# Performance work log

Measured on AMD Instinct MI355X. Metric: run time of the kernel, lower is better.

Reference implementation:

```python
import jax, jax.numpy as jnp
import numpy as np

N, E, IN, HID, OUT, H = 50000, 400000, 128, 32, 64, 4
HID_DIM = HID * H  # 128


def _param(key, shape, scale=0.05):
    return jax.random.normal(key, shape, dtype=jnp.float32) * scale


def setup_inputs() -> dict:
    key = jax.random.key(0)
    ks = jax.random.split(key, 32)
    inp = {
        "x": jax.random.normal(ks[0], (N, IN), dtype=jnp.float32),
        "edge_index": jax.random.randint(ks[1], (2, E), 0, N, dtype=jnp.int32),
        "edge_weight": jax.random.uniform(ks[2], (E,), dtype=jnp.float32),
        # layer 0: in=128 -> H=4, C=32, concat => 128
        "Wl0": _param(ks[3], (IN, H * HID)), "bl0": jnp.zeros((H * HID,), jnp.float32),
        "Wr0": _param(ks[4], (IN, H * HID)), "br0": jnp.zeros((H * HID,), jnp.float32),
        "We0": _param(ks[5], (1, H * HID)),
        "att0": _param(ks[6], (H, HID)),
        "b0": jnp.zeros((H * HID,), jnp.float32),
        "g0": jnp.ones((H * HID,), jnp.float32), "be0": jnp.zeros((H * HID,), jnp.float32),
        # layer 1: in=128 -> H=4, C=64, concat=False (mean over heads) => 64
        "Wl1": _param(ks[7], (HID_DIM, H * OUT)), "bl1": jnp.zeros((H * OUT,), jnp.float32),
        "Wr1": _param(ks[8], (HID_DIM, H * OUT)), "br1": jnp.zeros((H * OUT,), jnp.float32),
        "We1": _param(ks[9], (1, H * OUT)),
        "att1": _param(ks[10], (H, OUT)),
        "b1": jnp.zeros((OUT,), jnp.float32),
        "g1": jnp.ones((OUT,), jnp.float32), "be1": jnp.zeros((OUT,), jnp.float32),
        # residual projections
        "P0": _param(ks[11], (IN, HID_DIM)), "pb0": jnp.zeros((HID_DIM,), jnp.float32),
        "P1": _param(ks[12], (HID_DIM, OUT)), "pb1": jnp.zeros((OUT,), jnp.float32),
    }
    return inp


def _add_self_loops(src, dst, ew):
    # PyG add_self_loops with fill_value='mean': loop attr = mean of incoming edge attrs per node
    s = jax.ops.segment_sum(ew, dst, num_segments=N)
    cnt = jax.ops.segment_sum(jnp.ones_like(ew), dst, num_segments=N)
    loop_w = s / jnp.maximum(cnt, 1.0)
    idx = jnp.arange(N, dtype=src.dtype)
    return jnp.concatenate([src, idx]), jnp.concatenate([dst, idx]), jnp.concatenate([ew, loop_w])


def _gatv2_layer(x, src, dst, ew, Wl, bl, Wr, br, We, att, b, g, be, C, concat):
    xl = (x @ Wl + bl).reshape(N, H, C)  # source transform (lin_l)
    xr = (x @ Wr + br).reshape(N, H, C)  # target transform (lin_r)
    eattr = (ew[:, None] @ We).reshape(-1, H, C)
    e = jax.nn.leaky_relu(xl[src] + xr[dst] + eattr, 0.2)  # [E', H, C]
    logits = jnp.einsum('ehc,hc->eh', e, att)
    # segment softmax over target nodes
    m = jax.ops.segment_max(logits, dst, num_segments=N)
    p = jnp.exp(logits - m[dst])
    denom = jax.ops.segment_sum(p, dst, num_segments=N)
    alpha = p / denom[dst]
    out = jax.ops.segment_sum(xl[src] * alpha[..., None], dst, num_segments=N)  # [N, H, C]
    if concat:
        out = out.reshape(N, H * C) + b
    else:
        out = out.mean(axis=1) + b
    out = jax.nn.elu(out)
    mu = out.mean(-1, keepdims=True)
    var = out.var(-1, keepdims=True)
    return (out - mu) / jnp.sqrt(var + 1e-5) * g + be


def reference(x, edge_index, edge_weight,
              Wl0, bl0, Wr0, br0, We0, att0, b0, g0, be0,
              Wl1, bl1, Wr1, br1, We1, att1, b1, g1, be1,
              P0, pb0, P1, pb1):
    src, dst, ew = _add_self_loops(edge_index[0], edge_index[1], edge_weight)
    h = x
    h1 = _gatv2_layer(h, src, dst, ew, Wl0, bl0, Wr0, br0, We0, att0, b0, g0, be0, HID, True)
    h = h1 + (h @ P0 + pb0)
    h2 = _gatv2_layer(h, src, dst, ew, Wl1, bl1, Wr1, br1, We1, att1, b1, g1, be1, OUT, False)
    h = h2 + (h @ P1 + pb1)
    return h
```

## Files before the change

kernel.cpp:

```cpp
#include <hip/hip_runtime.h>
#include <math.h>

#define N_NODES 50000
#define N_EDGES 400000
#define NPAD    50176
#define MROWS   50048
#define HC0 128
#define HC1 256

typedef short    bf16x8 __attribute__((ext_vector_type(8)));
typedef float    f32x4  __attribute__((ext_vector_type(4)));
typedef _Float16 h2     __attribute__((ext_vector_type(2)));
typedef _Float16 h4     __attribute__((ext_vector_type(4)));
typedef _Float16 h8     __attribute__((ext_vector_type(8)));

__device__ inline unsigned short f2bf(float f) {
  union { float f; unsigned u; } v; v.f = f;
  unsigned r = v.u + 0x7FFFu + ((v.u >> 16) & 1u);
  return (unsigned short)(r >> 16);
}
__device__ inline h2 mkh2(float a, float b) {
  h2 r; r[0] = (_Float16)a; r[1] = (_Float16)b; return r;
}
__device__ inline float hdot2(h2 a, h2 b, float c) {
#if __has_builtin(__builtin_amdgcn_fdot2)
  return __builtin_amdgcn_fdot2(a, b, c, false);
#else
  return c + (float)a[0] * (float)b[0] + (float)a[1] * (float)b[1];
#endif
}

__global__ void deg_kernel(const int* __restrict__ ei, const float* __restrict__ ew,
                           float* __restrict__ s, int* __restrict__ deg) {
  int e = blockIdx.x * 256 + threadIdx.x;
  if (e < N_EDGES) {
    int dst = ei[N_EDGES + e];
    atomicAdd(&s[dst], ew[e]);
    atomicAdd(&deg[dst], 1);
  }
}

__global__ void scan1(const int* __restrict__ deg, int* __restrict__ part,
                      int* __restrict__ bsum) {
  int i = blockIdx.x * 256 + threadIdx.x;
  int lane = threadIdx.x & 63, wid = threadIdx.x >> 6;
  int v = (i < N_NODES) ? deg[i] + 1 : 0;
  int inc = v;
#pragma unroll
  for (int d = 1; d < 64; d <<= 1) { int y = __shfl_up(inc, d, 64); if (lane >= d) inc += y; }
  __shared__ int wsum[4];
  if (lane == 63) wsum[wid] = inc;
  __syncthreads();
  int off = 0;
#pragma unroll
  for (int w = 0; w < 4; ++w) { int sv = wsum[w]; if (w < wid) off += sv; }
  part[i] = inc - v + off;
  if (threadIdx.x == 0) bsum[blockIdx.x] = wsum[0] + wsum[1] + wsum[2] + wsum[3];
}

__global__ void scan2(int* __restrict__ bsum) {
  int t = threadIdx.x;
  int lane = t & 63, wid = t >> 6;
  int v = (t < 196) ? bsum[t] : 0;
  int inc = v;
#pragma unroll
  for (int d = 1; d < 64; d <<= 1) { int y = __shfl_up(inc, d, 64); if (lane >= d) inc += y; }
  __shared__ int wsum[4];
  if (lane == 63) wsum[wid] = inc;
  __syncthreads();
  int off = 0;
#pragma unroll
  for (int w = 0; w < 4; ++w) { int sv = wsum[w]; if (w < wid) off += sv; }
  if (t < 196) bsum[t] = inc - v + off;
}

__global__ void self_kernel(const float* __restrict__ s, const int* __restrict__ deg,
                            const int* __restrict__ part, const int* __restrict__ bsum,
                            int2* __restrict__ csr2) {
  int i = blockIdx.x * 256 + threadIdx.x;
  if (i >= N_NODES) return;
  float w = s[i] / fmaxf((float)deg[i], 1.0f);
  int start = part[i] + bsum[i >> 8];
  csr2[start] = make_int2(i, __float_as_int(w));
}

__global__ void scatter_kernel(const int* __restrict__ ei, const float* __restrict__ ew,
                               const int* __restrict__ part, const int* __restrict__ bsum,
                               int* __restrict__ cursor, int2* __restrict__ csr2) {
  int e = blockIdx.x * 256 + threadIdx.x;
  if (e >= N_EDGES) return;
  int dst = ei[N_EDGES + e];
  int pos = atomicAdd(&cursor[dst], 1);
  int idx = part[dst] + bsum[dst >> 8] + 1 + pos;
  csr2[idx] = make_int2(ei[e], __float_as_int(ew[e]));
}

__global__ void cvt_bf16(const float* __restrict__ in, unsigned short* __restrict__ out,
                         int n4) {
  int i = blockIdx.x * 256 + threadIdx.x;
  if (i >= n4) return;
  float4 v = ((const float4*)in)[i];
  ushort4 o; o.x = f2bf(v.x); o.y = f2bf(v.y); o.z = f2bf(v.z); o.w = f2bf(v.w);
  ((ushort4*)out)[i] = o;
}

__global__ void pack_w(const float* __restrict__ Wl0, const float* __restrict__ Wr0,
                       const float* __restrict__ P0,  const float* __restrict__ Wl1,
                       const float* __restrict__ Wr1, const float* __restrict__ P1,
                       unsigned short* __restrict__ o_wl0, unsigned short* __restrict__ o_wr0,
                       unsigned short* __restrict__ o_p0,  unsigned short* __restrict__ o_wl1,
                       unsigned short* __restrict__ o_wr1, unsigned short* __restrict__ o_p1) {
  int n = blockIdx.x, k = threadIdx.x;
  const float* W; unsigned short* O; int N, nl;
  if      (n < 128) { W = Wl0; O = o_wl0; N = 128; nl = n; }
  else if (n < 256) { W = Wr0; O = o_wr0; N = 128; nl = n - 128; }
  else if (n < 384) { W = P0;  O = o_p0;  N = 128; nl = n - 256; }
  else if (n < 640) { W = Wl1; O = o_wl1; N = 256; nl = n - 384; }
  else if (n < 896) { W = Wr1; O = o_wr1; N = 256; nl = n - 640; }
  else              { W = P1;  O = o_p1;  N = 64;  nl = n - 896; }
  O[nl * 128 + k] = f2bf(W[(size_t)k * N + nl]);
}

__global__ __launch_bounds__(256) void gemm_l0(
    const unsigned short* __restrict__ A, const unsigned short* __restrict__ BT,
    const float* __restrict__ bias0, const float* __restrict__ bias1,
    const float* __restrict__ bias2,
    _Float16* __restrict__ o_xl, _Float16* __restrict__ o_xr,
    float* __restrict__ o_h, int M) {
  __shared__ unsigned short As[64 * 136];
  const int tid = threadIdx.x;
  const int rbase = blockIdx.x * 64;
#pragma unroll
  for (int i = 0; i < 4; ++i) {
    int c = i * 256 + tid;
    int row = c >> 4, slot = c & 15;
    int ar = rbase + row; if (ar > M - 1) ar = M - 1;
    uint4 v = *(const uint4*)(A + (size_t)ar * 128 + slot * 8);
    *(uint4*)(As + row * 136 + slot * 8) = v;
  }
  __syncthreads();
  const int w = tid >> 6, l = tid & 63;
  const int lr = l & 15, lg = l >> 4;
#pragma unroll
  for (int i = 0; i < 6; ++i) {
    const int ct = w * 6 + i;
    const bf16x8* bp = (const bf16x8*)(BT + (size_t)(ct * 16 + lr) * 128 + lg * 8);
    bf16x8 b0 = bp[0], b1 = bp[4], b2 = bp[8], b3 = bp[12];
    const int colb = ct * 16 + lg * 4;
    const int cc = colb & 127;
    const float* bptr = (ct < 8 ? bias0 : (ct < 16 ? bias1 : bias2));
    float4 bv = *(const float4*)(bptr + cc);
#pragma unroll
    for (int rt = 0; rt < 4; ++rt) {
      const unsigned short* ap = As + (rt * 16 + lr) * 136 + lg * 8;
      bf16x8 a0 = *(const bf16x8*)(ap);
      bf16x8 a1 = *(const bf16x8*)(ap + 32);
      bf16x8 a2 = *(const bf16x8*)(ap + 64);
      bf16x8 a3 = *(const bf16x8*)(ap + 96);
      f32x4 acc = {0.f, 0.f, 0.f, 0.f};
      acc = __builtin_amdgcn_mfma_f32_16x16x32_bf16(b0, a0, acc, 0, 0, 0);
      acc = __builtin_amdgcn_mfma_f32_16x16x32_bf16(b1, a1, acc, 0, 0, 0);
      acc = __builtin_amdgcn_mfma_f32_16x16x32_bf16(b2, a2, acc, 0, 0, 0);
      acc = __builtin_amdgcn_mfma_f32_16x16x32_bf16(b3, a3, acc, 0, 0, 0);
      const int row = rbase + rt * 16 + lr;
      if (ct < 16) {
        h4 o;
        o[0] = (_Float16)(acc[0] + bv.x); o[1] = (_Float16)(acc[1] + bv.y);
        o[2] = (_Float16)(acc[2] + bv.z); o[3] = (_Float16)(acc[3] + bv.w);
        *(h4*)((ct < 8 ? o_xl : o_xr) + (size_t)row * 128 + cc) = o;
      } else {
        float4 o;
        o.x = acc[0] + bv.x; o.y = acc[1] + bv.y;
        o.z = acc[2] + bv.z; o.w = acc[3] + bv.w;
        *(float4*)(o_h + (size_t)row * 128 + cc) = o;
      }
    }
  }
}

__global__ __launch_bounds__(256) void gemm_l1(
    const unsigned short* __restrict__ A, const unsigned short* __restrict__ BT,
    const float* __restrict__ bias0, const float* __restrict__ bias1,
    const float* __restrict__ bias2,
    _Float16* __restrict__ o_xl, _Float16* __restrict__ o_xr,
    float* __restrict__ o_out, int M) {
  __shared__ unsigned short As[64 * 136];
  const int tid = threadIdx.x;
  const int rbase = blockIdx.x * 64;
#pragma unroll
  for (int i = 0; i < 4; ++i) {
    int c = i * 256 + tid;
    int row = c >> 4, slot = c & 15;
    int ar = rbase + row; if (ar > M - 1) ar = M - 1;
    uint4 v = *(const uint4*)(A + (size_t)ar * 128 + slot * 8);
    *(uint4*)(As + row * 136 + slot * 8) = v;
  }
  __syncthreads();
  const int w = tid >> 6, l = tid & 63;
  const int lr = l & 15, lg = l >> 4;
#pragma unroll
  for (int i = 0; i < 9; ++i) {
    const int ct = w * 9 + i;
    const bf16x8* bp = (const bf16x8*)(BT + (size_t)(ct * 16 + lr) * 128 + lg * 8);
    bf16x8 b0 = bp[0], b1 = bp[4], b2 = bp[8], b3 = bp[12];
    const int colb = ct * 16 + lg * 4;
    const int cc = (ct < 32) ? (colb & 255) : (colb - 512);
    const float* bptr = (ct < 16 ? bias0 : (ct < 32 ? bias1 : bias2));
    float4 bv = *(const float4*)(bptr + cc);
#pragma unroll
    for (int rt = 0; rt < 4; ++rt) {
      const unsigned short* ap = As + (rt * 16 + lr) * 136 + lg * 8;
      bf16x8 a0 = *(const bf16x8*)(ap);
      bf16x8 a1 = *(const bf16x8*)(ap + 32);
      bf16x8 a2 = *(const bf16x8*)(ap + 64);
      bf16x8 a3 = *(const bf16x8*)(ap + 96);
      f32x4 acc = {0.f, 0.f, 0.f, 0.f};
      acc = __builtin_amdgcn_mfma_f32_16x16x32_bf16(b0, a0, acc, 0, 0, 0);
      acc = __builtin_amdgcn_mfma_f32_16x16x32_bf16(b1, a1, acc, 0, 0, 0);
      acc = __builtin_amdgcn_mfma_f32_16x16x32_bf16(b2, a2, acc, 0, 0, 0);
      acc = __builtin_amdgcn_mfma_f32_16x16x32_bf16(b3, a3, acc, 0, 0, 0);
      const int row = rbase + rt * 16 + lr;
      if (ct < 32) {
        h4 o;
        o[0] = (_Float16)(acc[0] + bv.x); o[1] = (_Float16)(acc[1] + bv.y);
        o[2] = (_Float16)(acc[2] + bv.z); o[3] = (_Float16)(acc[3] + bv.w);
        *(h4*)((ct < 16 ? o_xl : o_xr) + (size_t)row * 256 + cc) = o;
      } else if (row < M) {
        float4 o;
        o.x = acc[0] + bv.x; o.y = acc[1] + bv.y;
        o.z = acc[2] + bv.z; o.w = acc[3] + bv.w;
        *(float4*)(o_out + (size_t)row * 64 + cc) = o;
      }
    }
  }
}

__device__ inline void edge_step0(int2 rec, h8 a8, bool valid,
                                  const h2* xrv2, const h2* wef2, const h2* att2,
                                  h2* acc2, float& den) {
  _Float16 wh = (_Float16)__int_as_float(rec.y);
  h2 w2; w2[0] = wh; w2[1] = wh;
  const h2 c02 = mkh2(0.2f, 0.2f);
  int4 ai = __builtin_bit_cast(int4, a8);
  h2 av[4];
  av[0] = __builtin_bit_cast(h2, ai.x); av[1] = __builtin_bit_cast(h2, ai.y);
  av[2] = __builtin_bit_cast(h2, ai.z); av[3] = __builtin_bit_cast(h2, ai.w);
  float c = 0.f;
#pragma unroll
  for (int k = 0; k < 4; ++k) {
    h2 sv = av[k] + (w2 * wef2[k] + xrv2[k]);
    h2 lk = __builtin_elementwise_max(sv, sv * c02);
    c = hdot2(lk, att2[k], c);
  }
  c += __shfl_xor(c, 1, 64); c += __shfl_xor(c, 2, 64);
  float p = valid ? __expf(c) : 0.f;
  den += p;
  _Float16 ph = (_Float16)p;
  h2 p2; p2[0] = ph; p2[1] = ph;
#pragma unroll
  for (int k = 0; k < 4; ++k) acc2[k] = p2 * av[k] + acc2[k];
}

__device__ inline void edge_step1(int2 rec, h8 a8, bool valid,
                                  const h2* xrv2, const h2* wef2, const h2* att2,
                                  h2* acc2, float& den) {
  _Float16 wh = (_Float16)__int_as_float(rec.y);
  h2 w2; w2[0] = wh; w2[1] = wh;
  const h2 c02 = mkh2(0.2f, 0.2f);
  int4 ai = __builtin_bit_cast(int4, a8);
  h2 av[4];
  av[0] = __builtin_bit_cast(h2, ai.x); av[1] = __builtin_bit_cast(h2, ai.y);
  av[2] = __builtin_bit_cast(h2, ai.z); av[3] = __builtin_bit_cast(h2, ai.w);
  float c = 0.f;
#pragma unroll
  for (int k = 0; k < 4; ++k) {
    h2 sv = av[k] + (w2 * wef2[k] + xrv2[k]);
    h2 lk = __builtin_elementwise_max(sv, sv * c02);
    c = hdot2(lk, att2[k], c);
  }
  c += __shfl_xor(c, 1, 64); c += __shfl_xor(c, 2, 64); c += __shfl_xor(c, 4, 64);
  float p = valid ? __expf(c) : 0.f;
  den += p;
  _Float16 ph = (_Float16)p;
  h2 p2; p2[0] = ph; p2[1] = ph;
#pragma unroll
  for (int k = 0; k < 4; ++k) acc2[k] = p2 * av[k] + acc2[k];
}

__global__ __launch_bounds__(256) void agg0(
    const int* __restrict__ part, const int* __restrict__ bsum,
    const int* __restrict__ deg, const int2* __restrict__ csr2,
    const _Float16* __restrict__ xl, const _Float16* __restrict__ xr,
    const float* __restrict__ We, const float* __restrict__ att,
    const float* __restrict__ b, const float* __restrict__ g,
    const float* __restrict__ be, const float* __restrict__ hres,
    unsigned short* __restrict__ hout) {
  const int wid = threadIdx.x >> 6, l = threadIdx.x & 63;
  const int n = blockIdx.x * 4 + wid;
  const int grp = l >> 4, cl = l & 15, c0 = cl * 8;
  h2 xrv2[4], wef2[4], att2[4];
  {
    h8 x8 = *(const h8*)(xr + (size_t)n * HC0 + c0);
    int4 xi = __builtin_bit_cast(int4, x8);
    xrv2[0] = __builtin_bit_cast(h2, xi.x); xrv2[1] = __builtin_bit_cast(h2, xi.y);
    xrv2[2] = __builtin_bit_cast(h2, xi.z); xrv2[3] = __builtin_bit_cast(h2, xi.w);
    float4 w0 = *(const float4*)(We + c0),  w1 = *(const float4*)(We + c0 + 4);
    float4 t0 = *(const float4*)(att + c0), t1 = *(const float4*)(att + c0 + 4);
    wef2[0] = mkh2(w0.x, w0.y); wef2[1] = mkh2(w0.z, w0.w);
    wef2[2] = mkh2(w1.x, w1.y); wef2[3] = mkh2(w1.z, w1.w);
    att2[0] = mkh2(t0.x, t0.y); att2[1] = mkh2(t0.z, t0.w);
    att2[2] = mkh2(t1.x, t1.y); att2[3] = mkh2(t1.z, t1.w);
  }
  const int start = part[n] + bsum[n >> 8];
  const int cnt   = deg[n] + 1;
  const int last  = start + cnt - 1;
  h2 acc2[4] = {};
  float den = 0.f;
#define IDX0(E) (start + (E) > last ? last : start + (E))
  int2 rA0 = csr2[IDX0(grp)],      rA1 = csr2[IDX0(grp + 4)];
  int2 rB0 = csr2[IDX0(grp + 8)],  rB1 = csr2[IDX0(grp + 12)];
  h8 aA0 = *(const h8*)(xl + (size_t)rA0.x * HC0 + c0);
  h8 aA1 = *(const h8*)(xl + (size_t)rA1.x * HC0 + c0);
  const int trips = (cnt + 7) >> 3;
  int e = grp;
  for (int t = 0; t < trips; ++t) {
    int2 rC0 = csr2[IDX0(e + 16)], rC1 = csr2[IDX0(e + 20)];
    h8 aB0 = *(const h8*)(xl + (size_t)rB0.x * HC0 + c0);
    h8 aB1 = *(const h8*)(xl + (size_t)rB1.x * HC0 + c0);
    edge_step0(rA0, aA0, e < cnt,     xrv2, wef2, att2, acc2, den);
    edge_step0(rA1, aA1, e + 4 < cnt, xrv2, wef2, att2, acc2, den);
    rA0 = rB0; rA1 = rB1; rB0 = rC0; rB1 = rC1; aA0 = aB0; aA1 = aB1;
    e += 8;
  }
#undef IDX0
  den += __shfl_xor(den, 16, 64); den += __shfl_xor(den, 32, 64);
#pragma unroll
  for (int k = 0; k < 4; ++k) {
    int b16 = __shfl_xor(__builtin_bit_cast(int, acc2[k]), 16, 64);
    acc2[k] = acc2[k] + __builtin_bit_cast(h2, b16);
    int b32 = __shfl_xor(__builtin_bit_cast(int, acc2[k]), 32, 64);
    acc2[k] = acc2[k] + __builtin_bit_cast(h2, b32);
  }
  float v[8], s1 = 0.f, s2 = 0.f;
  float dinv = 1.f / den;
  {
    float4 b0v = *(const float4*)(b + c0), b1v = *(const float4*)(b + c0 + 4);
    float bb[8] = {b0v.x,b0v.y,b0v.z,b0v.w,b1v.x,b1v.y,b1v.z,b1v.w};
#pragma unroll
    for (int j = 0; j < 8; ++j) {
      float t = (float)acc2[j >> 1][j & 1] * dinv + bb[j];
      t = t > 0.f ? t : __expf(t) - 1.f;
      v[j] = t; s1 += t; s2 += t * t;
    }
  }
  s1 += __shfl_xor(s1, 1, 64); s2 += __shfl_xor(s2, 1, 64);
  s1 += __shfl_xor(s1, 2, 64); s2 += __shfl_xor(s2, 2, 64);
  s1 += __shfl_xor(s1, 4, 64); s2 += __shfl_xor(s2, 4, 64);
  s1 += __shfl_xor(s1, 8, 64); s2 += __shfl_xor(s2, 8, 64);
  float mean = s1 * (1.f / 128.f);
  float inv  = rsqrtf(s2 * (1.f / 128.f) - mean * mean + 1e-5f);
  if (grp == 0) {
    float4 g0v = *(const float4*)(g + c0),  g1v = *(const float4*)(g + c0 + 4);
    float4 e0v = *(const float4*)(be + c0), e1v = *(const float4*)(be + c0 + 4);
    float4 h0v = *(const float4*)(hres + (size_t)n * HC0 + c0);
    float4 h1v = *(const float4*)(hres + (size_t)n * HC0 + c0 + 4);
    float gg[8] = {g0v.x,g0v.y,g0v.z,g0v.w,g1v.x,g1v.y,g1v.z,g1v.w};
    float ee[8] = {e0v.x,e0v.y,e0v.z,e0v.w,e1v.x,e1v.y,e1v.z,e1v.w};
    float hh[8] = {h0v.x,h0v.y,h0v.z,h0v.w,h1v.x,h1v.y,h1v.z,h1v.w};
    bf16x8 o;
#pragma unroll
    for (int j = 0; j < 8; ++j)
      o[j] = (short)f2bf((v[j] - mean) * inv * gg[j] + ee[j] + hh[j]);
    *(bf16x8*)(hout + (size_t)n * HC0 + c0) = o;
  }
}

__global__ __launch_bounds__(256) void agg1(
    const int* __restrict__ part, const int* __restrict__ bsum,
    const int* __restrict__ deg, const int2* __restrict__ csr2,
    const _Float16* __restrict__ xl, const _Float16* __restrict__ xr,
    const float* __restrict__ We, const float* __restrict__ att,
    const float* __restrict__ b, const float* __restrict__ g,
    const float* __restrict__ be, float* __restrict__ out) {
  const int wid = threadIdx.x >> 6, l = threadIdx.x & 63;
  const int n = blockIdx.x * 4 + wid;
  const int grp = l >> 5, cl = l & 31, c0 = cl * 8;
  h2 xrv2[4], wef2[4], att2[4];
  {
    h8 x8 = *(const h8*)(xr + (size_t)n * HC1 + c0);
    int4 xi = __builtin_bit_cast(int4, x8);
    xrv2[0] = __builtin_bit_cast(h2, xi.x); xrv2[1] = __builtin_bit_cast(h2, xi.y);
    xrv2[2] = __builtin_bit_cast(h2, xi.z); xrv2[3] = __builtin_bit_cast(h2, xi.w);
    float4 w0 = *(const float4*)(We + c0),  w1 = *(const float4*)(We + c0 + 4);
    float4 t0 = *(const float4*)(att + c0), t1 = *(const float4*)(att + c0 + 4);
    wef2[0] = mkh2(w0.x, w0.y); wef2[1] = mkh2(w0.z, w0.w);
    wef2[2] = mkh2(w1.x, w1.y); wef2[3] = mkh2(w1.z, w1.w);
    att2[0] = mkh2(t0.x, t0.y); att2[1] = mkh2(t0.z, t0.w);
    att2[2] = mkh2(t1.x, t1.y); att2[3] = mkh2(t1.z, t1.w);
  }
  const int start = part[n] + bsum[n >> 8];
  const int cnt   = deg[n] + 1;
  const int last  = start + cnt - 1;
  h2 acc2[4] = {};
  float den = 0.f;
#define IDX1(E) (start + (E) > last ? last : start + (E))
  int2 rA0 = csr2[IDX1(grp)],     rA1 = csr2[IDX1(grp + 2)];
  int2 rB0 = csr2[IDX1(grp + 4)], rB1 = csr2[IDX1(grp + 6)];
  h8 aA0 = *(const h8*)(xl + (size_t)rA0.x * HC1 + c0);
  h8 aA1 = *(const h8*)(xl + (size_t)rA1.x * HC1 + c0);
  const int trips = (cnt + 3) >> 2;
  int e = grp;
  for (int t = 0; t < trips; ++t) {
    int2 rC0 = csr2[IDX1(e + 8)], rC1 = csr2[IDX1(e + 10)];
    h8 aB0 = *(const h8*)(xl + (size_t)rB0.x * HC1 + c0);
    h8 aB1 = *(const h8*)(xl + (size_t)rB1.x * HC1 + c0);
    edge_step1(rA0, aA0, e < cnt,     xrv2, wef2, att2, acc2, den);
    edge_step1(rA1, aA1, e + 2 < cnt, xrv2, wef2, att2, acc2, den);
    rA0 = rB0; rA1 = rB1; rB0 = rC0; rB1 = rC1; aA0 = aB0; aA1 = aB1;
    e += 4;
  }
#undef IDX1
  den += __shfl_xor(den, 32, 64);
#pragma unroll
  for (int k = 0; k < 4; ++k) {
    int b32 = __shfl_xor(__builtin_bit_cast(int, acc2[k]), 32, 64);
    acc2[k] = acc2[k] + __builtin_bit_cast(h2, b32);
  }
  float dinv = 1.f / den;
  float v[8], s1 = 0.f, s2 = 0.f;
  const int oc = (cl & 7) * 8;
  {
    float4 b0v = *(const float4*)(b + oc), b1v = *(const float4*)(b + oc + 4);
    float bb[8] = {b0v.x,b0v.y,b0v.z,b0v.w,b1v.x,b1v.y,b1v.z,b1v.w};
#pragma unroll
    for (int j = 0; j < 8; ++j) {
      float t = (float)acc2[j >> 1][j & 1] * dinv;
      t += __shfl_xor(t, 8, 64);
      t += __shfl_xor(t, 16, 64);
      t = t * 0.25f + bb[j];
      t = t > 0.f ? t : __expf(t) - 1.f;
      v[j] = t; s1 += t; s2 += t * t;
    }
  }
  s1 += __shfl_xor(s1, 1, 64); s2 += __shfl_xor(s2, 1, 64);
  s1 += __shfl_xor(s1, 2, 64); s2 += __shfl_xor(s2, 2, 64);
  s1 += __shfl_xor(s1, 4, 64); s2 += __shfl_xor(s2, 4, 64);
  float mean = s1 * (1.f / 64.f);
  float inv  = rsqrtf(s2 * (1.f / 64.f) - mean * mean + 1e-5f);
  if (grp == 0 && cl < 8) {
    float4 g0v = *(const float4*)(g + oc),  g1v = *(const float4*)(g + oc + 4);
    float4 e0v = *(const float4*)(be + oc), e1v = *(const float4*)(be + oc + 4);
    float gg[8] = {g0v.x,g0v.y,g0v.z,g0v.w,g1v.x,g1v.y,g1v.z,g1v.w};
    float ee[8] = {e0v.x,e0v.y,e0v.z,e0v.w,e1v.x,e1v.y,e1v.z,e1v.w};
    float* po = out + (size_t)n * 64 + oc;
    float4 o0 = *(const float4*)po, o1 = *(const float4*)(po + 4);
    o0.x += (v[0] - mean) * inv * gg[0] + ee[0];
    o0.y += (v[1] - mean) * inv * gg[1] + ee[1];
    o0.z += (v[2] - mean) * inv * gg[2] + ee[2];
    o0.w += (v[3] - mean) * inv * gg[3] + ee[3];
    o1.x += (v[4] - mean) * inv * gg[4] + ee[4];
    o1.y += (v[5] - mean) * inv * gg[5] + ee[5];
    o1.z += (v[6] - mean) * inv * gg[6] + ee[6];
    o1.w += (v[7] - mean) * inv * gg[7] + ee[7];
    *(float4*)po = o0; *(float4*)(po + 4) = o1;
  }
}

extern "C" void kernel_launch(void* const* d_in, const int* in_sizes, int n_in,
                              void* d_out, int out_size, void* d_ws, size_t ws_size,
                              hipStream_t stream) {
  const float* x    = (const float*)d_in[0];
  const int*   ei   = (const int*)  d_in[1];
  const float* ew   = (const float*)d_in[2];
  const float* Wl0  = (const float*)d_in[3];
  const float* bl0  = (const float*)d_in[4];
  const float* Wr0  = (const float*)d_in[5];
  const float* br0  = (const float*)d_in[6];
  const float* We0  = (const float*)d_in[7];
  const float* att0 = (const float*)d_in[8];
  const float* b0   = (const float*)d_in[9];
  const float* g0   = (const float*)d_in[10];
  const float* be0  = (const float*)d_in[11];
  const float* Wl1  = (const float*)d_in[12];
  const float* bl1  = (const float*)d_in[13];
  const float* Wr1  = (const float*)d_in[14];
  const float* br1  = (const float*)d_in[15];
  const float* We1  = (const float*)d_in[16];
  const float* att1 = (const float*)d_in[17];
  const float* b1   = (const float*)d_in[18];
  const float* g1   = (const float*)d_in[19];
  const float* be1  = (const float*)d_in[20];
  const float* P0   = (const float*)d_in[21];
  const float* pb0  = (const float*)d_in[22];
  const float* P1   = (const float*)d_in[23];
  const float* pb1  = (const float*)d_in[24];
  float* out = (float*)d_out;

  float* f        = (float*)d_ws;
  float* s_loopw  = f;
  int*   deg      = (int*)(f + 50176);
  int*   cursor   = (int*)(f + 100352);
  int*   part     = (int*)(f + 150528);
  int*   bsum     = (int*)(f + 200704);
  int2*  csr2     = (int2*)(f + 200960);
  unsigned short* wl0T = (unsigned short*)(f + 1102080);
  unsigned short* wr0T = wl0T + 16384;
  unsigned short* p0T  = wl0T + 32768;
  unsigned short* wl1T = (unsigned short*)(f + 1126656);
  unsigned short* wr1T = wl1T + 32768;
  unsigned short* p1T  = wl1T + 65536;
  unsigned short* xb   = (unsigned short*)(f + 1163520);
  unsigned short* hb   = (unsigned short*)(f + 4366592);
  float*          hres = f + 7569664;
  _Float16*       RA   = (_Float16*)(f + 13975808);
  _Float16*       RB   = (_Float16*)(f + 20381952);
  _Float16* xl0h = RA, *xr0h = RB;
  _Float16* xl1h = RA, *xr1h = RB;

  hipMemsetAsync(s_loopw, 0, (size_t)(50176 * 3) * sizeof(float), stream);
  deg_kernel<<<(N_EDGES + 255) / 256, 256, 0, stream>>>(ei, ew, s_loopw, deg);
  scan1<<<NPAD / 256, 256, 0, stream>>>(deg, part, bsum);
  scan2<<<1, 256, 0, stream>>>(bsum);
  self_kernel<<<(N_NODES + 255) / 256, 256, 0, stream>>>(s_loopw, deg, part, bsum, csr2);
  scatter_kernel<<<(N_EDGES + 255) / 256, 256, 0, stream>>>(ei, ew, part, bsum,
                                                            cursor, csr2);

  cvt_bf16<<<(N_NODES * 128 / 4 + 255) / 256, 256, 0, stream>>>(x, xb, N_NODES * 128 / 4);
  pack_w<<<960, 128, 0, stream>>>(Wl0, Wr0, P0, Wl1, Wr1, P1,
                                  wl0T, wr0T, p0T, wl1T, wr1T, p1T);

  const int GB = MROWS / 64;
  gemm_l0<<<GB, 256, 0, stream>>>(xb, wl0T, bl0, br0, pb0, xl0h, xr0h, hres, N_NODES);
  agg0<<<N_NODES / 4, 256, 0, stream>>>(part, bsum, deg, csr2,
                                        xl0h, xr0h, We0, att0, b0, g0, be0, hres, hb);

  gemm_l1<<<GB, 256, 0, stream>>>(hb, wl1T, bl1, br1, pb1, xl1h, xr1h, out, N_NODES);
  agg1<<<N_NODES / 4, 256, 0, stream>>>(part, bsum, deg, csr2,
                                        xl1h, xr1h, We1, att1, b1, g1, be1, out);
}
```

Measured before the change: 228.1 us.

## Fuse bf16 input conversion into layer-0 GEMM and store residual in fp16

Removes the separate cvt_bf16 kernel; gemm_l0 now reads fp32 x directly and converts to bf16 while staging into shared memory. The residual projection output is stored as fp16 instead of fp32, halving its write and read traffic in agg0. Aggregation kernels drop per-edge index clamping, reading past the segment end instead, with a zeroed pad after the CSR array. This trades a small precision loss on the residual and relies on masked out-of-segment reads for correctness.

```diff
diff --git a/kernel.cpp b/kernel.cpp
--- a/kernel.cpp
+++ b/kernel.cpp
@@ -7,6 +7,7 @@
 #define MROWS   50048
 #define HC0 128
 #define HC1 256
+#define CSR_TOTAL (N_NODES + N_EDGES)
 
 typedef short    bf16x8 __attribute__((ext_vector_type(8)));
 typedef float    f32x4  __attribute__((ext_vector_type(4)));
@@ -93,15 +94,6 @@
   int pos = atomicAdd(&cursor[dst], 1);
   int idx = part[dst] + bsum[dst >> 8] + 1 + pos;
   csr2[idx] = make_int2(ei[e], __float_as_int(ew[e]));
-}
-
-__global__ void cvt_bf16(const float* __restrict__ in, unsigned short* __restrict__ out,
-                         int n4) {
-  int i = blockIdx.x * 256 + threadIdx.x;
-  if (i >= n4) return;
-  float4 v = ((const float4*)in)[i];
-  ushort4 o; o.x = f2bf(v.x); o.y = f2bf(v.y); o.z = f2bf(v.z); o.w = f2bf(v.w);
-  ((ushort4*)out)[i] = o;
 }
 
 __global__ void pack_w(const float* __restrict__ Wl0, const float* __restrict__ Wr0,
@@ -122,21 +114,22 @@
 }
 
 __global__ __launch_bounds__(256) void gemm_l0(
-    const unsigned short* __restrict__ A, const unsigned short* __restrict__ BT,
+    const float* __restrict__ X, const unsigned short* __restrict__ BT,
     const float* __restrict__ bias0, const float* __restrict__ bias1,
     const float* __restrict__ bias2,
     _Float16* __restrict__ o_xl, _Float16* __restrict__ o_xr,
-    float* __restrict__ o_h, int M) {
+    _Float16* __restrict__ o_h, int M) {
   __shared__ unsigned short As[64 * 136];
   const int tid = threadIdx.x;
   const int rbase = blockIdx.x * 64;
 #pragma unroll
-  for (int i = 0; i < 4; ++i) {
+  for (int i = 0; i < 8; ++i) {
     int c = i * 256 + tid;
-    int row = c >> 4, slot = c & 15;
+    int row = c >> 5, c4 = c & 31;
     int ar = rbase + row; if (ar > M - 1) ar = M - 1;
-    uint4 v = *(const uint4*)(A + (size_t)ar * 128 + slot * 8);
-    *(uint4*)(As + row * 136 + slot * 8) = v;
+    float4 v = *(const float4*)(X + (size_t)ar * 128 + c4 * 4);
+    ushort4 o; o.x = f2bf(v.x); o.y = f2bf(v.y); o.z = f2bf(v.z); o.w = f2bf(v.w);
+    *(ushort4*)(As + row * 136 + c4 * 4) = o;
   }
   __syncthreads();
   const int w = tid >> 6, l = tid & 63;
@@ -163,17 +156,11 @@
       acc = __builtin_amdgcn_mfma_f32_16x16x32_bf16(b2, a2, acc, 0, 0, 0);
       acc = __builtin_amdgcn_mfma_f32_16x16x32_bf16(b3, a3, acc, 0, 0, 0);
       const int row = rbase + rt * 16 + lr;
-      if (ct < 16) {
-        h4 o;
-        o[0] = (_Float16)(acc[0] + bv.x); o[1] = (_Float16)(acc[1] + bv.y);
-        o[2] = (_Float16)(acc[2] + bv.z); o[3] = (_Float16)(acc[3] + bv.w);
-        *(h4*)((ct < 8 ? o_xl : o_xr) + (size_t)row * 128 + cc) = o;
-      } else {
-        float4 o;
-        o.x = acc[0] + bv.x; o.y = acc[1] + bv.y;
-        o.z = acc[2] + bv.z; o.w = acc[3] + bv.w;
-        *(float4*)(o_h + (size_t)row * 128 + cc) = o;
-      }
+      h4 o;
+      o[0] = (_Float16)(acc[0] + bv.x); o[1] = (_Float16)(acc[1] + bv.y);
+      o[2] = (_Float16)(acc[2] + bv.z); o[3] = (_Float16)(acc[3] + bv.w);
+      _Float16* dst = (ct < 8) ? o_xl : (ct < 16 ? o_xr : o_h);
+      *(h4*)(dst + (size_t)row * 128 + cc) = o;
     }
   }
 }
@@ -293,7 +280,7 @@
     const _Float16* __restrict__ xl, const _Float16* __restrict__ xr,
     const float* __restrict__ We, const float* __restrict__ att,
     const float* __restrict__ b, const float* __restrict__ g,
-    const float* __restrict__ be, const float* __restrict__ hres,
+    const float* __restrict__ be, const _Float16* __restrict__ hres,
     unsigned short* __restrict__ hout) {
   const int wid = threadIdx.x >> 6, l = threadIdx.x & 63;
   const int n = blockIdx.x * 4 + wid;
@@ -313,18 +300,17 @@
   }
   const int start = part[n] + bsum[n >> 8];
   const int cnt   = deg[n] + 1;
-  const int last  = start + cnt - 1;
+  const int2* seg = csr2 + start;
   h2 acc2[4] = {};
   float den = 0.f;
-#define IDX0(E) (start + (E) > last ? last : start + (E))
-  int2 rA0 = csr2[IDX0(grp)],      rA1 = csr2[IDX0(grp + 4)];
-  int2 rB0 = csr2[IDX0(grp + 8)],  rB1 = csr2[IDX0(grp + 12)];
+  int2 rA0 = seg[grp],      rA1 = seg[grp + 4];
+  int2 rB0 = seg[grp + 8],  rB1 = seg[grp + 12];
   h8 aA0 = *(const h8*)(xl + (size_t)rA0.x * HC0 + c0);
   h8 aA1 = *(const h8*)(xl + (size_t)rA1.x * HC0 + c0);
   const int trips = (cnt + 7) >> 3;
   int e = grp;
   for (int t = 0; t < trips; ++t) {
-    int2 rC0 = csr2[IDX0(e + 16)], rC1 = csr2[IDX0(e + 20)];
+    int2 rC0 = seg[e + 16], rC1 = seg[e + 20];
     h8 aB0 = *(const h8*)(xl + (size_t)rB0.x * HC0 + c0);
     h8 aB1 = *(const h8*)(xl + (size_t)rB1.x * HC0 + c0);
     edge_step0(rA0, aA0, e < cnt,     xrv2, wef2, att2, acc2, den);
@@ -332,7 +318,6 @@
     rA0 = rB0; rA1 = rB1; rB0 = rC0; rB1 = rC1; aA0 = aB0; aA1 = aB1;
     e += 8;
   }
-#undef IDX0
   den += __shfl_xor(den, 16, 64); den += __shfl_xor(den, 32, 64);
 #pragma unroll
   for (int k = 0; k < 4; ++k) {
@@ -362,15 +347,13 @@
   if (grp == 0) {
     float4 g0v = *(const float4*)(g + c0),  g1v = *(const float4*)(g + c0 + 4);
     float4 e0v = *(const float4*)(be + c0), e1v = *(const float4*)(be + c0 + 4);
-    float4 h0v = *(const float4*)(hres + (size_t)n * HC0 + c0);
-    float4 h1v = *(const float4*)(hres + (size_t)n * HC0 + c0 + 4);
+    h8 hh = *(const h8*)(hres + (size_t)n * HC0 + c0);
     float gg[8] = {g0v.x,g0v.y,g0v.z,g0v.w,g1v.x,g1v.y,g1v.z,g1v.w};
     float ee[8] = {e0v.x,e0v.y,e0v.z,e0v.w,e1v.x,e1v.y,e1v.z,e1v.w};
-    float hh[8] = {h0v.x,h0v.y,h0v.z,h0v.w,h1v.x,h1v.y,h1v.z,h1v.w};
     bf16x8 o;
 #pragma unroll
     for (int j = 0; j < 8; ++j)
-      o[j] = (short)f2bf((v[j] - mean) * inv * gg[j] + ee[j] + hh[j]);
+      o[j] = (short)f2bf((v[j] - mean) * inv * gg[j] + ee[j] + (float)hh[j]);
     *(bf16x8*)(hout + (size_t)n * HC0 + c0) = o;
   }
 }
@@ -400,18 +383,17 @@
   }
   const int start = part[n] + bsum[n >> 8];
   const int cnt   = deg[n] + 1;
-  const int last  = start + cnt - 1;
+  const int2* seg = csr2 + start;
   h2 acc2[4] = {};
   float den = 0.f;
-#define IDX1(E) (start + (E) > last ? last : start + (E))
-  int2 rA0 = csr2[IDX1(grp)],     rA1 = csr2[IDX1(grp + 2)];
-  int2 rB0 = csr2[IDX1(grp + 4)], rB1 = csr2[IDX1(grp + 6)];
+  int2 rA0 = seg[grp],     rA1 = seg[grp + 2];
+  int2 rB0 = seg[grp + 4], rB1 = seg[grp + 6];
   h8 aA0 = *(const h8*)(xl + (size_t)rA0.x * HC1 + c0);
   h8 aA1 = *(const h8*)(xl + (size_t)rA1.x * HC1 + c0);
   const int trips = (cnt + 3) >> 2;
   int e = grp;
   for (int t = 0; t < trips; ++t) {
-    int2 rC0 = csr2[IDX1(e + 8)], rC1 = csr2[IDX1(e + 10)];
+    int2 rC0 = seg[e + 8], rC1 = seg[e + 10];
     h8 aB0 = *(const h8*)(xl + (size_t)rB0.x * HC1 + c0);
     h8 aB1 = *(const h8*)(xl + (size_t)rB1.x * HC1 + c0);
     edge_step1(rA0, aA0, e < cnt,     xrv2, wef2, att2, acc2, den);
@@ -419,7 +401,6 @@
     rA0 = rB0; rA1 = rB1; rB0 = rC0; rB1 = rC1; aA0 = aB0; aA1 = aB1;
     e += 4;
   }
-#undef IDX1
   den += __shfl_xor(den, 32, 64);
 #pragma unroll
   for (int k = 0; k < 4; ++k) {
@@ -509,15 +490,15 @@
   unsigned short* wl1T = (unsigned short*)(f + 1126656);
   unsigned short* wr1T = wl1T + 32768;
   unsigned short* p1T  = wl1T + 65536;
-  unsigned short* xb   = (unsigned short*)(f + 1163520);
-  unsigned short* hb   = (unsigned short*)(f + 4366592);
-  float*          hres = f + 7569664;
-  _Float16*       RA   = (_Float16*)(f + 13975808);
-  _Float16*       RB   = (_Float16*)(f + 20381952);
+  unsigned short* hb   = (unsigned short*)(f + 1163520);
+  _Float16*       hres = (_Float16*)(f + 4366592);
+  _Float16*       RA   = (_Float16*)(f + 7569664);
+  _Float16*       RB   = (_Float16*)(f + 13975808);
   _Float16* xl0h = RA, *xr0h = RB;
   _Float16* xl1h = RA, *xr1h = RB;
 
   hipMemsetAsync(s_loopw, 0, (size_t)(50176 * 3) * sizeof(float), stream);
+  hipMemsetAsync(csr2 + CSR_TOTAL, 0, 64 * sizeof(int2), stream);
   deg_kernel<<<(N_EDGES + 255) / 256, 256, 0, stream>>>(ei, ew, s_loopw, deg);
   scan1<<<NPAD / 256, 256, 0, stream>>>(deg, part, bsum);
   scan2<<<1, 256, 0, stream>>>(bsum);
@@ -525,12 +506,11 @@
   scatter_kernel<<<(N_EDGES + 255) / 256, 256, 0, stream>>>(ei, ew, part, bsum,
                                                             cursor, csr2);
 
-  cvt_bf16<<<(N_NODES * 128 / 4 + 255) / 256, 256, 0, stream>>>(x, xb, N_NODES * 128 / 4);
   pack_w<<<960, 128, 0, stream>>>(Wl0, Wr0, P0, Wl1, Wr1, P1,
                                   wl0T, wr0T, p0T, wl1T, wr1T, p1T);
 
   const int GB = MROWS / 64;
-  gemm_l0<<<GB, 256, 0, stream>>>(xb, wl0T, bl0, br0, pb0, xl0h, xr0h, hres, N_NODES);
+  gemm_l0<<<GB, 256, 0, stream>>>(x, wl0T, bl0, br0, pb0, xl0h, xr0h, hres, N_NODES);
   agg0<<<N_NODES / 4, 256, 0, stream>>>(part, bsum, deg, csr2,
                                         xl0h, xr0h, We0, att0, b0, g0, be0, hres, hb);
 
```

Result: faster. 223.3 us (-2.1%).
